# Performance work log

Hardware: AMD Instinct MI355X
Metric: run time of the kernel (lower is better)

## Reference

```python
import jax, jax.numpy as jnp
import numpy as np

jax.config.update("jax_enable_x64", True)  # hash math needs int64 (prime * coord > 2^31)

LEVEL = 16
MOD_T = 2 ** 16
FDIM = 3
_PRIMES = (1, 2654435761, 805459861)  # first feature_dim primes from the module


def _grid_sizes():
    # mirrors torch float32 computation: b = exp((log(n_max)-log(n_min))/(level-1))
    n_min = np.float32(4.0)
    n_max = np.float32(256.0)
    b = np.float32(np.exp((np.log(n_max) - np.log(n_min)) / np.float32(LEVEL - 1)))
    return [int(n_min * b ** i) for i in range(LEVEL)]


def setup_inputs() -> dict:
    key = jax.random.key(0)
    k1, k2 = jax.random.split(key)
    images = jax.random.uniform(k1, (16, 3, 256, 256), dtype=jnp.float32)
    hash_table = (jax.random.uniform(k2, (LEVEL, MOD_T, FDIM), dtype=jnp.float32)
                  * 0.0002 - 0.0001)
    return {"images": images, "hash_table": hash_table}


def reference(images, hash_table):
    b, c, h, w = images.shape
    primes = jnp.array(_PRIMES[:FDIM], dtype=jnp.int64)
    neg_inf = jnp.array(-jnp.inf, dtype=images.dtype)
    outs = []
    for lvl, grid in enumerate(_grid_sizes()):
        kh, kw = h // grid, w // grid
        # max_pool2d(images*grid, kernel=(kh,kw), stride=(kh,kw))
        pooled = jax.lax.reduce_window(
            images * grid, neg_inf, jax.lax.max,
            window_dimensions=(1, 1, kh, kw),
            window_strides=(1, 1, kh, kw),
            padding="VALID")                     # [B, F, gh, gw]
        idx = pooled.astype(jnp.int64) * primes[None, :, None, None]
        g = idx[:, 0]
        for i in range(1, FDIM):
            g = g ^ idx[:, i]
        g = g % MOD_T                             # [B, gh, gw]
        f = hash_table[lvl][g]                    # gather -> [B, gh, gw, F]
        f = jnp.transpose(f, (0, 3, 1, 2))        # [B, F, gh, gw]
        # F.interpolate(..., mode='bilinear') == half-pixel, align_corners=False
        f = jax.image.resize(f, (b, FDIM, h, w), method="bilinear")
        outs.append(f)
    return jnp.concatenate(outs, axis=1)          # [B, level*F, H, W]
```

## Files before the change

### kernel.cpp

```cpp
#include <hip/hip_runtime.h>
#include <stdint.h>
#include <math.h>


#define NLVL 16
#define NB   16

__constant__ int   c_P[NLVL]   = {4,5,6,9,12,15,21,28,36,51,64,85,128,256,256,256};
__constant__ float c_G[NLVL]   = {4.f,5.f,6.f,9.f,12.f,15.f,21.f,27.f,36.f,48.f,63.f,84.f,111.f,147.f,194.f,255.f};
__constant__ int   c_CUM[14]   = {0,16,41,77,158,302,527,968,1752,3048,5649,9745,16970,33354};

#define CELLS_PB   33354
#define CELLS_TOT  (CELLS_PB*NB)
#define TASKS_TOT  7424
#define POOL_BLOCKS (TASKS_TOT/4)
#define DIR_BLOCKS  1024
#define K1_BLOCKS   (POOL_BLOCKS + DIR_BLOCKS)
#define TILE_BLOCKS (13*16*16)

__device__ __forceinline__ uint32_t hash3(float m0, float m1, float m2, float g) {
    uint32_t v0 = (uint32_t)(int)(m0 * g);
    uint32_t v1 = (uint32_t)(int)(m1 * g);
    uint32_t v2 = (uint32_t)(int)(m2 * g);
    return (v0 ^ (v1 * 2654435761u) ^ (v2 * 805459861u)) & 0xFFFFu;
}

__device__ __forceinline__ float4 max4(float4 a, float4 b) {
    float4 r;
    r.x = fmaxf(a.x, b.x); r.y = fmaxf(a.y, b.y);
    r.z = fmaxf(a.z, b.z); r.w = fmaxf(a.w, b.w);
    return r;
}

__global__ __launch_bounds__(256) void pool_direct(const float* __restrict__ img,
                                                   const float* __restrict__ tab,
                                                   float* __restrict__ mws,
                                                   float* __restrict__ out)
{
    static constexpr int K_P[13]     = {4,5,6,9,12,15,21,28,36,51,64,85,128};
    static constexpr int K_KH[13]    = {64,51,42,28,21,17,12,9,7,5,4,3,2};
    static constexpr int K_CUM[13]   = {0,16,41,77,158,302,527,968,1752,3048,5649,9745,16970};
    static constexpr int K_ROW16[13] = {0,64,144,240,384,576,816,1152,1600,2176,2992,4016,5376};

    __shared__ float4 sw[4][3][64];

    if (blockIdx.x >= POOL_BLOCKS) {
        int t = (blockIdx.x - POOL_BLOCKS) * 256 + threadIdx.x;
        int b = t >> 14;
        int pix0 = (t & 16383) << 2;
        const float* p = img + (size_t)b * 196608 + pix0;
        float4 i0 = *(const float4*)p;
        float4 i1 = *(const float4*)(p + 65536);
        float4 i2 = *(const float4*)(p + 131072);
#pragma unroll
        for (int lvl = 13; lvl < 16; ++lvl) {
            float g = c_G[lvl];
            const float* T = tab + (size_t)lvl * 196608;
            uint32_t g0 = hash3(i0.x, i1.x, i2.x, g);
            uint32_t g1 = hash3(i0.y, i1.y, i2.y, g);
            uint32_t g2 = hash3(i0.z, i1.z, i2.z, g);
            uint32_t g3 = hash3(i0.w, i1.w, i2.w, g);
            float3 f0 = *(const float3*)(T + g0 * 3);
            float3 f1 = *(const float3*)(T + g1 * 3);
            float3 f2 = *(const float3*)(T + g2 * 3);
            float3 f3 = *(const float3*)(T + g3 * 3);
            float4 o0, o1, o2;
            o0.x = f0.x; o1.x = f0.y; o2.x = f0.z;
            o0.y = f1.x; o1.y = f1.y; o2.y = f1.z;
            o0.z = f2.x; o1.z = f2.y; o2.z = f2.z;
            o0.w = f3.x; o1.w = f3.y; o2.w = f3.z;
            float* ob = out + ((size_t)b * 48 + 3 * lvl) * 65536 + pix0;
            *(float4*)ob            = o0;
            *(float4*)(ob + 65536)  = o1;
            *(float4*)(ob + 131072) = o2;
        }
        return;
    }

    int wid  = threadIdx.x >> 6;
    int lane = threadIdx.x & 63;
    int task = (blockIdx.x << 2) + wid;

    int lvl = 0;
#pragma unroll
    for (int l = 1; l < 13; ++l) lvl += (task >= K_ROW16[l]);
    int P = K_P[lvl], kh = K_KH[lvl];
    int rem = task - K_ROW16[lvl];
    int b   = rem / P;
    int cr  = rem - b * P;

    const float4* rp = (const float4*)(img + (size_t)b * 196608) + (size_t)(cr * kh) * 64 + lane;
    float4 cm0 = make_float4(-INFINITY, -INFINITY, -INFINITY, -INFINITY);
    float4 cm1 = cm0, cm2 = cm0;
    for (int r = 0; r < kh; ++r, rp += 64) {
        cm0 = max4(cm0, rp[0]);
        cm1 = max4(cm1, rp[16384]);
        cm2 = max4(cm2, rp[32768]);
    }
    sw[wid][0][lane] = cm0;
    sw[wid][1][lane] = cm1;
    sw[wid][2][lane] = cm2;
    __syncthreads();

    const float* f0 = (const float*)&sw[wid][0][0];
    const float* f1 = (const float*)&sw[wid][1][0];
    const float* f2 = (const float*)&sw[wid][2][0];
    for (int cx = lane; cx < P; cx += 64) {
        float m0 = -INFINITY, m1 = -INFINITY, m2 = -INFINITY;
        int cb = cx * kh;
        for (int c = cb; c < cb + kh; ++c) {
            m0 = fmaxf(m0, f0[c]);
            m1 = fmaxf(m1, f1[c]);
            m2 = fmaxf(m2, f2[c]);
        }
        int idx = K_CUM[lvl] * NB + b * P * P + cr * P + cx;
        mws[idx]                 = m0;
        mws[idx + CELLS_TOT]     = m1;
        mws[idx + 2 * CELLS_TOT] = m2;
    }
}

__global__ __launch_bounds__(256) void render_tiles(const float* __restrict__ tab,
                                                    const float* __restrict__ mws,
                                                    float* __restrict__ out)
{
    __shared__ float4 s[34 * 34];
    int blk   = blockIdx.x;
    int tile  = blk & 15;
    int plane = blk >> 4;
    int lvl   = plane >> 4;
    int b     = plane & 15;
    int P     = c_P[lvl];
    int yt0   = (tile >> 2) * 64;
    int xt0   = (tile & 3) * 64;

    int nlo  = ((2 * yt0 + 1) * P - 256) >> 9;
    int r_lo = nlo < 0 ? 0 : (nlo > P - 1 ? P - 1 : nlo);
    int nhi  = (((2 * (yt0 + 63) + 1) * P - 256) >> 9) + 1;
    int r_hi = nhi < 0 ? 0 : (nhi > P - 1 ? P - 1 : nhi);
    int mlo  = ((2 * xt0 + 1) * P - 256) >> 9;
    int c_lo = mlo < 0 ? 0 : (mlo > P - 1 ? P - 1 : mlo);
    int mhi  = (((2 * (xt0 + 63) + 1) * P - 256) >> 9) + 1;
    int c_hi = mhi < 0 ? 0 : (mhi > P - 1 ? P - 1 : mhi);
    int span_y = r_hi - r_lo + 1;
    int span_x = c_hi - c_lo + 1;

    int planebase = c_CUM[lvl] * NB + b * P * P;
    const float* T = tab + (size_t)lvl * 196608;
    float gmul = c_G[lvl];
    int n = span_y * span_x;
    for (int t = threadIdx.x; t < n; t += 256) {
        int r = t / span_x, c = t - r * span_x;
        int idx = planebase + (r_lo + r) * P + c_lo + c;
        float m0 = mws[idx];
        float m1 = mws[idx + CELLS_TOT];
        float m2 = mws[idx + 2 * CELLS_TOT];
        uint32_t g = hash3(m0, m1, m2, gmul);
        float3 tv = *(const float3*)(T + g * 3);
        float4 fv; fv.x = tv.x; fv.y = tv.y; fv.z = tv.z; fv.w = 0.f;
        s[t] = fv;
    }
    __syncthreads();

    int lane = threadIdx.x & 63;
    int w    = threadIdx.x >> 6;
    int xq   = lane & 15;
    int rg   = lane >> 4;
    int xb   = xt0 + xq * 4;

    int ix0t[4], ix1t[4]; float wx0t[4], wx1t[4];
#pragma unroll
    for (int j = 0; j < 4; ++j) {
        int numx = (2 * (xb + j) + 1) * P - 256;
        int ix0  = numx >> 9;
        float fx = (float)(numx & 511) * (1.0f / 512.0f);
        int ix1;
        if (ix0 < 0)           { ix0 = 0;     ix1 = 0;     fx = 0.f; }
        else if (ix0 >= P - 1) { ix0 = P - 1; ix1 = P - 1; fx = 0.f; }
        else                   { ix1 = ix0 + 1; }
        ix0t[j] = ix0 - c_lo; ix1t[j] = ix1 - c_lo; wx1t[j] = fx; wx0t[j] = 1.f - fx;
    }

    int cur0 = -1, cur1 = -1;
    float r0v[3][4], r1v[3][4];

#pragma unroll
    for (int k = 0; k < 4; ++k) {
        int y = yt0 + w * 16 + rg * 4 + k;
        int numy = (2 * y + 1) * P - 256;
        int iy0  = numy >> 9;
        float fy = (float)(numy & 511) * (1.0f / 512.0f);
        int iy1;
        if (iy0 < 0)           { iy0 = 0;     iy1 = 0;     fy = 0.f; }
        else if (iy0 >= P - 1) { iy0 = P - 1; iy1 = P - 1; fy = 0.f; }
        else                   { iy1 = iy0 + 1; }

        if (iy0 != cur0) {
            if (iy0 == cur1) {
#pragma unroll
                for (int j = 0; j < 4; ++j) {
                    r0v[0][j] = r1v[0][j]; r0v[1][j] = r1v[1][j]; r0v[2][j] = r1v[2][j];
                }
            } else {
                const float4* p0 = s + (iy0 - r_lo) * span_x;
#pragma unroll
                for (int j = 0; j < 4; ++j) {
                    float4 a = p0[ix0t[j]], q = p0[ix1t[j]];
                    r0v[0][j] = wx0t[j] * a.x + wx1t[j] * q.x;
                    r0v[1][j] = wx0t[j] * a.y + wx1t[j] * q.y;
                    r0v[2][j] = wx0t[j] * a.z + wx1t[j] * q.z;
                }
            }
            cur0 = iy0;
        }
        if (iy1 != cur1) {
            if (iy1 == cur0 && iy1 == iy0) {
#pragma unroll
                for (int j = 0; j < 4; ++j) {
                    r1v[0][j] = r0v[0][j]; r1v[1][j] = r0v[1][j]; r1v[2][j] = r0v[2][j];
                }
            } else {
                const float4* p1 = s + (iy1 - r_lo) * span_x;
#pragma unroll
                for (int j = 0; j < 4; ++j) {
                    float4 a = p1[ix0t[j]], q = p1[ix1t[j]];
                    r1v[0][j] = wx0t[j] * a.x + wx1t[j] * q.x;
                    r1v[1][j] = wx0t[j] * a.y + wx1t[j] * q.y;
                    r1v[2][j] = wx0t[j] * a.z + wx1t[j] * q.z;
                }
            }
            cur1 = iy1;
        }

        float wy1 = fy, wy0 = 1.f - fy;
        float* o = out + ((size_t)b * 48 + 3 * lvl) * 65536 + (size_t)y * 256 + xb;
#pragma unroll
        for (int c = 0; c < 3; ++c) {
            float4 q;
            q.x = wy0 * r0v[c][0] + wy1 * r1v[c][0];
            q.y = wy0 * r0v[c][1] + wy1 * r1v[c][1];
            q.z = wy0 * r0v[c][2] + wy1 * r1v[c][2];
            q.w = wy0 * r0v[c][3] + wy1 * r1v[c][3];
            *(float4*)(o + (size_t)c * 65536) = q;
        }
    }
}

extern "C" void kernel_launch(void* const* d_in, const int* in_sizes, int n_in,
                              void* d_out, int out_size, void* d_ws, size_t ws_size,
                              hipStream_t stream)
{
    const float* img = (const float*)d_in[0];
    const float* tab = (const float*)d_in[1];
    float* out = (float*)d_out;
    float* mws = (float*)d_ws;

    hipLaunchKernelGGL(pool_direct,  dim3(K1_BLOCKS), dim3(256), 0, stream, img, tab, mws, out);
    hipLaunchKernelGGL(render_tiles, dim3(TILE_BLOCKS), dim3(256), 0, stream, tab, mws, out);
}
```

Baseline: 89.73 us.

## Pool coarse levels with one wave per cell and a shuffle reduction

The max-pool work is split into three block groups. Coarse levels 0-7 now use one wavefront per output cell, with lanes striding the kh×kh window and a cross-lane shuffle max reduction. Finer levels 8-12 keep the earlier row-band scheme, and the direct-hash path for levels 13-15 is unchanged. The aim is to spread the long serial row loops of large-window levels over many more waves for better load balance. The cost is non-coalesced scalar loads across window rows and far more waves in total.

```diff
diff --git a/kernel.cpp b/kernel.cpp
--- a/kernel.cpp
+++ b/kernel.cpp
@@ -12,10 +12,12 @@
 
 #define CELLS_PB   33354
 #define CELLS_TOT  (CELLS_PB*NB)
-#define TASKS_TOT  7424
-#define POOL_BLOCKS (TASKS_TOT/4)
-#define DIR_BLOCKS  1024
-#define K1_BLOCKS   (POOL_BLOCKS + DIR_BLOCKS)
+#define A_WAVES    28032
+#define A_BLOCKS   (A_WAVES/4)
+#define B_WAVES    5824
+#define B_BLOCKS   (B_WAVES/4)
+#define C_BLOCKS   1024
+#define K1_BLOCKS  (A_BLOCKS + B_BLOCKS + C_BLOCKS)
 #define TILE_BLOCKS (13*16*16)
 
 __device__ __forceinline__ uint32_t hash3(float m0, float m1, float m2, float g) {
@@ -37,86 +39,129 @@
                                                    float* __restrict__ mws,
                                                    float* __restrict__ out)
 {
-    static constexpr int K_P[13]     = {4,5,6,9,12,15,21,28,36,51,64,85,128};
-    static constexpr int K_KH[13]    = {64,51,42,28,21,17,12,9,7,5,4,3,2};
-    static constexpr int K_CUM[13]   = {0,16,41,77,158,302,527,968,1752,3048,5649,9745,16970};
-    static constexpr int K_ROW16[13] = {0,64,144,240,384,576,816,1152,1600,2176,2992,4016,5376};
-
-    __shared__ float4 sw[4][3][64];
-
-    if (blockIdx.x >= POOL_BLOCKS) {
-        int t = (blockIdx.x - POOL_BLOCKS) * 256 + threadIdx.x;
-        int b = t >> 14;
-        int pix0 = (t & 16383) << 2;
-        const float* p = img + (size_t)b * 196608 + pix0;
-        float4 i0 = *(const float4*)p;
-        float4 i1 = *(const float4*)(p + 65536);
-        float4 i2 = *(const float4*)(p + 131072);
-#pragma unroll
-        for (int lvl = 13; lvl < 16; ++lvl) {
-            float g = c_G[lvl];
-            const float* T = tab + (size_t)lvl * 196608;
-            uint32_t g0 = hash3(i0.x, i1.x, i2.x, g);
-            uint32_t g1 = hash3(i0.y, i1.y, i2.y, g);
-            uint32_t g2 = hash3(i0.z, i1.z, i2.z, g);
-            uint32_t g3 = hash3(i0.w, i1.w, i2.w, g);
-            float3 f0 = *(const float3*)(T + g0 * 3);
-            float3 f1 = *(const float3*)(T + g1 * 3);
-            float3 f2 = *(const float3*)(T + g2 * 3);
-            float3 f3 = *(const float3*)(T + g3 * 3);
-            float4 o0, o1, o2;
-            o0.x = f0.x; o1.x = f0.y; o2.x = f0.z;
-            o0.y = f1.x; o1.y = f1.y; o2.y = f1.z;
-            o0.z = f2.x; o1.z = f2.y; o2.z = f2.z;
-            o0.w = f3.x; o1.w = f3.y; o2.w = f3.z;
-            float* ob = out + ((size_t)b * 48 + 3 * lvl) * 65536 + pix0;
-            *(float4*)ob            = o0;
-            *(float4*)(ob + 65536)  = o1;
-            *(float4*)(ob + 131072) = o2;
+    static constexpr int A_P[8]    = {4,5,6,9,12,15,21,28};
+    static constexpr int A_KH[8]   = {64,51,42,28,21,17,12,9};
+    static constexpr int A_CUMC[9] = {0,16,41,77,158,302,527,968,1752};
+    static constexpr int B_P[5]    = {36,51,64,85,128};
+    static constexpr int B_KH[5]   = {7,5,4,3,2};
+    static constexpr int B_CUMR[6] = {0,36,87,151,236,364};
+    static constexpr int K_CUM[13] = {0,16,41,77,158,302,527,968,1752,3048,5649,9745,16970};
+
+    __shared__ float4 swc[4][3][64];
+
+    if (blockIdx.x < A_BLOCKS) {
+        int wv   = (blockIdx.x << 2) + (threadIdx.x >> 6);
+        int lane = threadIdx.x & 63;
+        int b    = wv / 1752;
+        int r    = wv - b * 1752;
+        int lvl  = 0;
+#pragma unroll
+        for (int l = 1; l < 8; ++l) lvl += (r >= A_CUMC[l]);
+        int P = A_P[lvl], kh = A_KH[lvl];
+        int cell = r - A_CUMC[lvl];
+        int cy = cell / P, cx = cell - cy * P;
+
+        const float* w0 = img + (size_t)b * 196608 + (size_t)(cy * kh) * 256 + cx * kh;
+        int n  = kh * kh;
+        int rr = lane / kh, cc = lane - rr * kh;
+        int q  = 64 / kh, rmd = 64 - q * kh;
+        float m0 = -INFINITY, m1 = -INFINITY, m2 = -INFINITY;
+        for (int i = lane; i < n; i += 64) {
+            int o = rr * 256 + cc;
+            m0 = fmaxf(m0, w0[o]);
+            m1 = fmaxf(m1, w0[65536 + o]);
+            m2 = fmaxf(m2, w0[131072 + o]);
+            rr += q; cc += rmd;
+            if (cc >= kh) { cc -= kh; ++rr; }
+        }
+#pragma unroll
+        for (int off = 32; off > 0; off >>= 1) {
+            m0 = fmaxf(m0, __shfl_xor(m0, off, 64));
+            m1 = fmaxf(m1, __shfl_xor(m1, off, 64));
+            m2 = fmaxf(m2, __shfl_xor(m2, off, 64));
+        }
+        if (lane == 0) {
+            int idx = K_CUM[lvl] * NB + b * P * P + cell;
+            mws[idx]                 = m0;
+            mws[idx + CELLS_TOT]     = m1;
+            mws[idx + 2 * CELLS_TOT] = m2;
         }
         return;
     }
 
-    int wid  = threadIdx.x >> 6;
-    int lane = threadIdx.x & 63;
-    int task = (blockIdx.x << 2) + wid;
-
-    int lvl = 0;
-#pragma unroll
-    for (int l = 1; l < 13; ++l) lvl += (task >= K_ROW16[l]);
-    int P = K_P[lvl], kh = K_KH[lvl];
-    int rem = task - K_ROW16[lvl];
-    int b   = rem / P;
-    int cr  = rem - b * P;
-
-    const float4* rp = (const float4*)(img + (size_t)b * 196608) + (size_t)(cr * kh) * 64 + lane;
-    float4 cm0 = make_float4(-INFINITY, -INFINITY, -INFINITY, -INFINITY);
-    float4 cm1 = cm0, cm2 = cm0;
-    for (int r = 0; r < kh; ++r, rp += 64) {
-        cm0 = max4(cm0, rp[0]);
-        cm1 = max4(cm1, rp[16384]);
-        cm2 = max4(cm2, rp[32768]);
-    }
-    sw[wid][0][lane] = cm0;
-    sw[wid][1][lane] = cm1;
-    sw[wid][2][lane] = cm2;
-    __syncthreads();
-
-    const float* f0 = (const float*)&sw[wid][0][0];
-    const float* f1 = (const float*)&sw[wid][1][0];
-    const float* f2 = (const float*)&sw[wid][2][0];
-    for (int cx = lane; cx < P; cx += 64) {
-        float m0 = -INFINITY, m1 = -INFINITY, m2 = -INFINITY;
-        int cb = cx * kh;
-        for (int c = cb; c < cb + kh; ++c) {
-            m0 = fmaxf(m0, f0[c]);
-            m1 = fmaxf(m1, f1[c]);
-            m2 = fmaxf(m2, f2[c]);
-        }
-        int idx = K_CUM[lvl] * NB + b * P * P + cr * P + cx;
-        mws[idx]                 = m0;
-        mws[idx + CELLS_TOT]     = m1;
-        mws[idx + 2 * CELLS_TOT] = m2;
+    if (blockIdx.x < A_BLOCKS + B_BLOCKS) {
+        int wid  = threadIdx.x >> 6;
+        int lane = threadIdx.x & 63;
+        int wv   = ((blockIdx.x - A_BLOCKS) << 2) + wid;
+        int b    = wv / 364;
+        int r    = wv - b * 364;
+        int li   = 0;
+#pragma unroll
+        for (int l = 1; l < 5; ++l) li += (r >= B_CUMR[l]);
+        int lvl = 8 + li;
+        int P = B_P[li], kh = B_KH[li];
+        int cr = r - B_CUMR[li];
+
+        const float4* rp = (const float4*)(img + (size_t)b * 196608) + (size_t)(cr * kh) * 64 + lane;
+        float4 cm0 = make_float4(-INFINITY, -INFINITY, -INFINITY, -INFINITY);
+        float4 cm1 = cm0, cm2 = cm0;
+        for (int rr = 0; rr < kh; ++rr, rp += 64) {
+            cm0 = max4(cm0, rp[0]);
+            cm1 = max4(cm1, rp[16384]);
+            cm2 = max4(cm2, rp[32768]);
+        }
+        swc[wid][0][lane] = cm0;
+        swc[wid][1][lane] = cm1;
+        swc[wid][2][lane] = cm2;
+        __syncthreads();
+
+        const float* f0 = (const float*)&swc[wid][0][0];
+        const float* f1 = (const float*)&swc[wid][1][0];
+        const float* f2 = (const float*)&swc[wid][2][0];
+        for (int cx = lane; cx < P; cx += 64) {
+            float m0 = -INFINITY, m1 = -INFINITY, m2 = -INFINITY;
+            int cb = cx * kh;
+            for (int c = cb; c < cb + kh; ++c) {
+                m0 = fmaxf(m0, f0[c]);
+                m1 = fmaxf(m1, f1[c]);
+                m2 = fmaxf(m2, f2[c]);
+            }
+            int idx = K_CUM[lvl] * NB + b * P * P + cr * P + cx;
+            mws[idx]                 = m0;
+            mws[idx + CELLS_TOT]     = m1;
+            mws[idx + 2 * CELLS_TOT] = m2;
+        }
+        return;
+    }
+
+    int t = (blockIdx.x - A_BLOCKS - B_BLOCKS) * 256 + threadIdx.x;
+    int b = t >> 14;
+    int pix0 = (t & 16383) << 2;
+    const float* p = img + (size_t)b * 196608 + pix0;
+    float4 i0 = *(const float4*)p;
+    float4 i1 = *(const float4*)(p + 65536);
+    float4 i2 = *(const float4*)(p + 131072);
+#pragma unroll
+    for (int lvl = 13; lvl < 16; ++lvl) {
+        float g = c_G[lvl];
+        const float* T = tab + (size_t)lvl * 196608;
+        uint32_t g0 = hash3(i0.x, i1.x, i2.x, g);
+        uint32_t g1 = hash3(i0.y, i1.y, i2.y, g);
+        uint32_t g2 = hash3(i0.z, i1.z, i2.z, g);
+        uint32_t g3 = hash3(i0.w, i1.w, i2.w, g);
+        float3 f0 = *(const float3*)(T + g0 * 3);
+        float3 f1 = *(const float3*)(T + g1 * 3);
+        float3 f2 = *(const float3*)(T + g2 * 3);
+        float3 f3 = *(const float3*)(T + g3 * 3);
+        float4 o0, o1, o2;
+        o0.x = f0.x; o1.x = f0.y; o2.x = f0.z;
+        o0.y = f1.x; o1.y = f1.y; o2.y = f1.z;
+        o0.z = f2.x; o1.z = f2.y; o2.z = f2.z;
+        o0.w = f3.x; o1.w = f3.y; o2.w = f3.z;
+        float* ob = out + ((size_t)b * 48 + 3 * lvl) * 65536 + pix0;
+        *(float4*)ob            = o0;
+        *(float4*)(ob + 65536)  = o1;
+        *(float4*)(ob + 131072) = o2;
     }
 }
 
```

Measured after the change: 91.89 us. 2.4% more time.
